# Kernel tuning notes

Hardware: AMD Instinct MI355X
Metric: run time of the kernel (lower is better)

The kernel has to match this reference:

```python
import jax, jax.numpy as jnp
import numpy as np

N = 100000      # nodes
E = 800000      # edges (avg degree 8)
F = 5           # num_node_features
D = 128         # embed_dim
H = 4           # heads
HD = D // H     # per-head dim = 32
H1, H2 = 64, 128  # mlp hidden dims


def _mlp(x, W1, b1, W2, b2, W3, b3):
    h = jax.nn.relu(x @ W1 + b1)
    h = jax.nn.relu(h @ W2 + b2)
    return h @ W3 + b3


def setup_inputs() -> dict:
    key = jax.random.key(0)
    ks = jax.random.split(key, 24)
    g = lambda i, shape: (jax.random.normal(ks[i], shape, dtype=jnp.float32) * 0.05)
    z = lambda d: jnp.zeros((d,), dtype=jnp.float32)
    return {
        "x": jax.random.normal(ks[0], (N, F), dtype=jnp.float32),
        "edge_index": jax.random.randint(ks[1], (2, E), 0, N),
        # mlp_prep: F -> 64 -> 128 -> D
        "prep_W1": g(2, (F, H1)),  "prep_b1": z(H1),
        "prep_W2": g(3, (H1, H2)), "prep_b2": z(H2),
        "prep_W3": g(4, (H2, D)),  "prep_b3": z(D),
        # mlp_update: D -> 64 -> 128 -> D
        "upd_W1": g(5, (D, H1)),   "upd_b1": z(H1),
        "upd_W2": g(6, (H1, H2)),  "upd_b2": z(H2),
        "upd_W3": g(7, (H2, D)),   "upd_b3": z(D),
        # TransformerConv projections (heads=4, per-head 32, concat -> D)
        "q_W": g(8, (D, D)),  "q_b": z(D),
        "k_W": g(9, (D, D)),  "k_b": z(D),
        "v_W": g(10, (D, D)), "v_b": z(D),
        "skip_W": g(11, (D, D)), "skip_b": z(D),
    }


def _transformer_conv(x, edge_index, q_W, q_b, k_W, k_b, v_W, v_b, skip_W, skip_b):
    # PyG TransformerConv: messages flow src=edge_index[0] -> dst=edge_index[1]
    src, dst = edge_index[0], edge_index[1]
    q = (x @ q_W + q_b).reshape(N, H, HD)
    k = (x @ k_W + k_b).reshape(N, H, HD)
    v = (x @ v_W + v_b).reshape(N, H, HD)
    scale = 1.0 / np.sqrt(HD).astype(np.float32)
    # per-edge attention logits [E, H]
    score = jnp.einsum('ehd,ehd->eh', q[dst], k[src]) * scale
    # segment softmax over incoming edges of each destination node
    m = jax.ops.segment_max(score, dst, num_segments=N)          # [N, H]
    e = jnp.exp(score - m[dst])                                  # [E, H]
    denom = jax.ops.segment_sum(e, dst, num_segments=N)         # [N, H]
    alpha = e / denom[dst]                                       # [E, H]
    # scatter-aggregate weighted values
    agg = jax.ops.segment_sum(alpha[..., None] * v[src], dst, num_segments=N)  # [N, H, HD]
    return agg.reshape(N, H * HD) + (x @ skip_W + skip_b)


def reference(x, edge_index,
              prep_W1, prep_b1, prep_W2, prep_b2, prep_W3, prep_b3,
              upd_W1, upd_b1, upd_W2, upd_b2, upd_W3, upd_b3,
              q_W, q_b, k_W, k_b, v_W, v_b, skip_W, skip_b):
    h_init = _mlp(x, prep_W1, prep_b1, prep_W2, prep_b2, prep_W3, prep_b3)
    h = _transformer_conv(h_init, edge_index, q_W, q_b, k_W, k_b, v_W, v_b, skip_W, skip_b)
    return h + _mlp(h, upd_W1, upd_b1, upd_W2, upd_b2, upd_W3, upd_b3)
```

## Files before the change

### kernel.cpp

```cpp
#include <hip/hip_runtime.h>
#include <hip/hip_bf16.h>

#define N_  100000
#define F_  5
#define D_  128
#define H_  4
#define HD_ 32
#define E_  800000

typedef __attribute__((ext_vector_type(8))) short bf16x8;
typedef __attribute__((ext_vector_type(4))) float f32x4;

__device__ __forceinline__ unsigned short f2bf(float f) {
  unsigned u = __float_as_uint(f);
  u += 0x7FFF + ((u >> 16) & 1);
  return (unsigned short)(u >> 16);
}

__device__ __forceinline__ unsigned pk2(float a, float b) {
  __hip_bfloat162 h = __float22bfloat162_rn(make_float2(a, b));
  return *(unsigned*)&h;
}

__device__ __forceinline__ float2 bf2f2(unsigned u) {
  float2 r;
  r.x = __uint_as_float(u << 16);
  r.y = __uint_as_float(u & 0xffff0000u);
  return r;
}

__device__ __forceinline__ float rowsum8(float x) {
  x += __int_as_float(__builtin_amdgcn_update_dpp(0, __float_as_int(x), 0x0B1, 0xF, 0xF, false));
  x += __int_as_float(__builtin_amdgcn_update_dpp(0, __float_as_int(x), 0x04E, 0xF, 0xF, false));
  x += __int_as_float(__builtin_amdgcn_update_dpp(0, __float_as_int(x), 0x141, 0xF, 0xF, false));
  return x;
}

template<int K, int M>
__device__ __forceinline__ void wconv_one(const float* __restrict__ W,
                                          unsigned short* __restrict__ WT,
                                          int idx) {
  const int r = idx & 7;
  const int l = (idx >> 3) & 15;
  const int rest = idx >> 7;
  const int kq = rest % (K / 8);
  const int i  = rest / (K / 8);
  WT[idx] = f2bf(W[(kq * 8 + r) * M + i * 16 + l]);
}

#define WCONV_NB 480
#define SCAN_NB ((N_ + 255) / 256)

__global__ __launch_bounds__(256) void k_wconv_all(
    const float* __restrict__ w0, const float* __restrict__ w1,
    const float* __restrict__ w2, const float* __restrict__ w3,
    const float* __restrict__ w4, const float* __restrict__ w5,
    const float* __restrict__ w6, const float* __restrict__ w7,
    const float* __restrict__ w8, unsigned short* __restrict__ WT,
    int* __restrict__ deg)
{
  if (blockIdx.x >= WCONV_NB) {
    const int i = (blockIdx.x - WCONV_NB) * 256 + threadIdx.x;
    if (i < N_) deg[i] = 0;
    return;
  }
  const int idx = blockIdx.x * 256 + threadIdx.x;
  if (idx < 8192)        wconv_one<64, 128>(w0, WT,          idx);
  else if (idx < 24576)  wconv_one<128,128>(w1, WT + 8192,   idx - 8192);
  else if (idx < 40960)  wconv_one<128,128>(w2, WT + 24576,  idx - 24576);
  else if (idx < 57344)  wconv_one<128,128>(w3, WT + 40960,  idx - 40960);
  else if (idx < 73728)  wconv_one<128,128>(w4, WT + 57344,  idx - 57344);
  else if (idx < 90112)  wconv_one<128,128>(w5, WT + 73728,  idx - 73728);
  else if (idx < 98304)  wconv_one<128, 64>(w6, WT + 90112,  idx - 90112);
  else if (idx < 106496) wconv_one<64, 128>(w7, WT + 98304,  idx - 98304);
  else                   wconv_one<128,128>(w8, WT + 106496, idx - 106496);
}

template<int K, int M>
__device__ __forceinline__ void gemm_frag(const unsigned short* sX,
                                          const unsigned short* __restrict__ WT,
                                          f32x4 (*acc)[4],
                                          int wr, int wc, int l16, int kg)
{
  constexpr int SX = K + 8;
  constexpr int IF = M / 32;
  #pragma unroll
  for (int i = 0; i < IF; ++i)
    #pragma unroll
    for (int j = 0; j < 4; ++j) acc[i][j] = (f32x4){0.f, 0.f, 0.f, 0.f};
  #pragma unroll
  for (int k0 = 0; k0 < K; k0 += 32) {
    const int kq = k0 / 8 + kg;
    bf16x8 aw[IF];
    #pragma unroll
    for (int i = 0; i < IF; ++i)
      aw[i] = *(const bf16x8*)&WT[(((wr * IF + i) * (K / 8) + kq) * 16 + l16) * 8];
    #pragma unroll
    for (int j = 0; j < 4; ++j) {
      const bf16x8 bx = *(const bf16x8*)&sX[(wc * 64 + j * 16 + l16) * SX + k0 + kg * 8];
      #pragma unroll
      for (int i = 0; i < IF; ++i)
        acc[i][j] = __builtin_amdgcn_mfma_f32_16x16x32_bf16(aw[i], bx, acc[i][j], 0, 0, 0);
    }
  }
}

template<int M, bool RELU, int SXO>
__device__ __forceinline__ void acc_to_lds(unsigned short* sY, f32x4 (*acc)[4],
                                           const float* __restrict__ bias,
                                           int wr, int wc, int l16, int kg)
{
  constexpr int IF = M / 32;
  float4 b4[IF];
  #pragma unroll
  for (int i = 0; i < IF; ++i)
    b4[i] = *(const float4*)&bias[(wr * IF + i) * 16 + kg * 4];
  #pragma unroll
  for (int j = 0; j < 4; ++j) {
    const int row = wc * 64 + j * 16 + l16;
    #pragma unroll
    for (int i = 0; i < IF; ++i) {
      const int f0 = (wr * IF + i) * 16 + kg * 4;
      float ox = acc[i][j][0] + b4[i].x, oy = acc[i][j][1] + b4[i].y;
      float oz = acc[i][j][2] + b4[i].z, ow = acc[i][j][3] + b4[i].w;
      if constexpr (RELU) {
        ox = fmaxf(ox, 0.f); oy = fmaxf(oy, 0.f);
        oz = fmaxf(oz, 0.f); ow = fmaxf(ow, 0.f);
      }
      uint2 p;
      p.x = pk2(ox, oy);
      p.y = pk2(oz, ow);
      *(uint2*)&sY[row * SXO + f0] = p;
    }
  }
}

__global__ __launch_bounds__(256) void k_prep_proj(
    const float* __restrict__ x,
    const float* __restrict__ pW1, const float* __restrict__ pb1,
    const unsigned short* __restrict__ wt_p2, const float* __restrict__ pb2,
    const unsigned short* __restrict__ wt_p3, const float* __restrict__ pb3,
    const unsigned short* __restrict__ wt_q, const float* __restrict__ qb,
    const unsigned short* __restrict__ wt_k, const float* __restrict__ kb,
    const unsigned short* __restrict__ wt_v, const float* __restrict__ vb,
    const unsigned short* __restrict__ wt_s, const float* __restrict__ sb,
    unsigned short* __restrict__ q16, unsigned short* __restrict__ k16,
    unsigned short* __restrict__ v16, float* __restrict__ out)
{
  __shared__ __align__(16) unsigned short bufA[128 * 72];
  __shared__ __align__(16) unsigned short bufB[128 * 136];

  const int t = threadIdx.x;
  const int node0 = blockIdx.x * 128;
  const int lane = t & 63;
  const int w  = t >> 6;
  const int wr = w >> 1, wc = w & 1;
  const int l16 = lane & 15, kg = lane >> 4;

  float* sxs = (float*)bufB;
  float* sw1 = (float*)bufB + 640;
  {
    const long gbase = (long)node0 * F_;
    for (int i = t; i < 128 * F_; i += 256) {
      const long g = gbase + i;
      sxs[i] = (g < (long)N_ * F_) ? x[g] : 0.f;
    }
    for (int i = t; i < 384; i += 256)
      sw1[i] = (i < 320) ? pW1[i] : pb1[i - 320];
  }
  __syncthreads();

  {
    const int n = t >> 1;
    const int half = (t & 1) * 32;
    float xr[F_];
    #pragma unroll
    for (int k = 0; k < F_; ++k) xr[k] = sxs[n * F_ + k];
    const float* sb1 = sw1 + 320;
    #pragma unroll
    for (int q = 0; q < 8; ++q) {
      float o[4];
      #pragma unroll
      for (int jj = 0; jj < 4; ++jj) {
        const int f = half + q * 4 + jj;
        float a = sb1[f];
        #pragma unroll
        for (int k = 0; k < F_; ++k) a = fmaf(xr[k], sw1[k * 64 + f], a);
        o[jj] = fmaxf(a, 0.f);
      }
      uint2 pkd;
      pkd.x = pk2(o[0], o[1]);
      pkd.y = pk2(o[2], o[3]);
      *(uint2*)&bufA[n * 72 + half + q * 4] = pkd;
    }
  }
  __syncthreads();

  f32x4 acc[4][4];

  gemm_frag<64, 128>(bufA, wt_p2, acc, wr, wc, l16, kg);
  acc_to_lds<128, true, 136>(bufB, acc, pb2, wr, wc, l16, kg);
  __syncthreads();

  gemm_frag<128, 128>(bufB, wt_p3, acc, wr, wc, l16, kg);
  __syncthreads();
  acc_to_lds<128, false, 136>(bufB, acc, pb3, wr, wc, l16, kg);
  __syncthreads();

  {
    const unsigned short* wtsP[3] = {wt_q, wt_k, wt_v};
    const float* bsP[3] = {qb, kb, vb};
    unsigned short* ysP[3] = {q16, k16, v16};
    #pragma unroll
    for (int ws = 0; ws < 3; ++ws) {
      gemm_frag<128, 128>(bufB, wtsP[ws], acc, wr, wc, l16, kg);
      const float* __restrict__ bias = bsP[ws];
      unsigned short* __restrict__ Yb = ysP[ws];
      float4 b4[4];
      #pragma unroll
      for (int i = 0; i < 4; ++i)
        b4[i] = *(const float4*)&bias[(wr * 4 + i) * 16 + kg * 4];
      #pragma unroll
      for (int j = 0; j < 4; ++j) {
        const int node = node0 + wc * 64 + j * 16 + l16;
        if (node >= N_) continue;
        #pragma unroll
        for (int i = 0; i < 4; ++i) {
          const int f0 = (wr * 4 + i) * 16 + kg * 4;
          uint2 ob;
          ob.x = pk2(acc[i][j][0] + b4[i].x, acc[i][j][1] + b4[i].y);
          ob.y = pk2(acc[i][j][2] + b4[i].z, acc[i][j][3] + b4[i].w);
          *(uint2*)&Yb[(long)node * D_ + f0] = ob;
        }
      }
    }
  }

  gemm_frag<128, 128>(bufB, wt_s, acc, wr, wc, l16, kg);
  {
    float4 b4[4];
    #pragma unroll
    for (int i = 0; i < 4; ++i)
      b4[i] = *(const float4*)&sb[(wr * 4 + i) * 16 + kg * 4];
    #pragma unroll
    for (int j = 0; j < 4; ++j) {
      const int node = node0 + wc * 64 + j * 16 + l16;
      if (node >= N_) continue;
      #pragma unroll
      for (int i = 0; i < 4; ++i) {
        const int f0 = (wr * 4 + i) * 16 + kg * 4;
        float4 o = make_float4(acc[i][j][0] + b4[i].x, acc[i][j][1] + b4[i].y,
                               acc[i][j][2] + b4[i].z, acc[i][j][3] + b4[i].w);
        *(float4*)&out[(long)node * D_ + f0] = o;
      }
    }
  }
}

__global__ __launch_bounds__(256) void k_update(
    const unsigned short* __restrict__ wt_u1, const float* __restrict__ ub1,
    const unsigned short* __restrict__ wt_u2, const float* __restrict__ ub2,
    const unsigned short* __restrict__ wt_u3, const float* __restrict__ ub3,
    float* __restrict__ out)
{
  __shared__ __align__(16) unsigned short bufA[128 * 72];
  __shared__ __align__(16) unsigned short bufB[128 * 136];

  const int t = threadIdx.x;
  const int node0 = blockIdx.x * 128;
  const int lane = t & 63;
  const int w  = t >> 6;
  const int wr = w >> 1, wc = w & 1;
  const int l16 = lane & 15, kg = lane >> 4;

  #pragma unroll
  for (int i = 0; i < 16; ++i) {
    const int g = t + 256 * i;
    const int row = g >> 5;
    const int kc  = g & 31;
    const int node = node0 + row;
    float4 xv = (node < N_) ? ((const float4*)out)[(long)node * 32 + kc]
                            : make_float4(0.f, 0.f, 0.f, 0.f);
    uint2 p;
    p.x = pk2(xv.x, xv.y);
    p.y = pk2(xv.z, xv.w);
    *(uint2*)&bufB[row * 136 + kc * 4] = p;
  }
  __syncthreads();

  f32x4 acc[4][4];

  gemm_frag<128, 64>(bufB, wt_u1, acc, wr, wc, l16, kg);
  acc_to_lds<64, true, 72>(bufA, acc, ub1, wr, wc, l16, kg);
  __syncthreads();

  gemm_frag<64, 128>(bufA, wt_u2, acc, wr, wc, l16, kg);
  acc_to_lds<128, true, 136>(bufB, acc, ub2, wr, wc, l16, kg);
  __syncthreads();

  gemm_frag<128, 128>(bufB, wt_u3, acc, wr, wc, l16, kg);
  {
    float4 b4[4];
    #pragma unroll
    for (int i = 0; i < 4; ++i)
      b4[i] = *(const float4*)&ub3[(wr * 4 + i) * 16 + kg * 4];
    #pragma unroll
    for (int j = 0; j < 4; ++j) {
      const int node = node0 + wc * 64 + j * 16 + l16;
      if (node >= N_) continue;
      #pragma unroll
      for (int i = 0; i < 4; ++i) {
        const int f0 = (wr * 4 + i) * 16 + kg * 4;
        const float4 r = *(const float4*)&out[(long)node * D_ + f0];
        float4 o = make_float4(acc[i][j][0] + b4[i].x + r.x,
                               acc[i][j][1] + b4[i].y + r.y,
                               acc[i][j][2] + b4[i].z + r.z,
                               acc[i][j][3] + b4[i].w + r.w);
        *(float4*)&out[(long)node * D_ + f0] = o;
      }
    }
  }
}

__global__ __launch_bounds__(256) void k_hist(const int* __restrict__ ei,
                                              int* __restrict__ deg) {
  int e = blockIdx.x * 256 + threadIdx.x;
  if (e < E_) atomicAdd(&deg[ei[E_ + e]], 1);
}

__global__ __launch_bounds__(256) void k_scan1(const int* __restrict__ deg,
                                               int* __restrict__ off,
                                               int* __restrict__ bsum) {
  __shared__ int s[256];
  const int t = threadIdx.x;
  const int i = blockIdx.x * 256 + t;
  const int v = (i < N_) ? deg[i] : 0;
  s[t] = v;
  __syncthreads();
  #pragma unroll
  for (int o = 1; o < 256; o <<= 1) {
    int u = (t >= o) ? s[t - o] : 0;
    __syncthreads();
    s[t] += u;
    __syncthreads();
  }
  if (i < N_) off[i] = s[t] - v;
  if (t == 255) bsum[blockIdx.x] = s[255];
}

__global__ __launch_bounds__(256) void k_scan23(const int* __restrict__ off,
                                                const int* __restrict__ bsum,
                                                int* __restrict__ cur,
                                                const int* __restrict__ deg,
                                                int2* __restrict__ meta) {
  __shared__ int sacc[256];
  const int t = threadIdx.x;
  const int bid = blockIdx.x;
  int s = 0;
  for (int j = t; j < bid; j += 256) s += bsum[j];
  sacc[t] = s;
  __syncthreads();
  #pragma unroll
  for (int o = 128; o > 0; o >>= 1) {
    if (t < o) sacc[t] += sacc[t + o];
    __syncthreads();
  }
  const int prefix = sacc[0];
  const int i = bid * 256 + t;
  if (i < N_) {
    const int o = off[i] + prefix;
    cur[i] = o;
    meta[i] = make_int2(o, deg[i]);
  }
}

__global__ __launch_bounds__(256) void k_fill(const int* __restrict__ ei,
                                              int* __restrict__ cur,
                                              int* __restrict__ esrc) {
  int e = blockIdx.x * 256 + threadIdx.x;
  if (e < E_) {
    int src = ei[e], dst = ei[E_ + e];
    int pos = atomicAdd(&cur[dst], 1);
    esrc[pos] = src;
  }
}

__global__ __launch_bounds__(256) void k_attn(
    const int* __restrict__ esrc, const int2* __restrict__ meta,
    const unsigned short* __restrict__ q,
    const unsigned short* __restrict__ kbuf,
    const unsigned short* __restrict__ vbuf,
    float* __restrict__ out)
{
  const int node = blockIdx.x * 4 + (threadIdx.x >> 6);
  const int lane = threadIdx.x & 63;
  if (node >= N_) return;

  const int2 md = meta[node];
  const int start = md.x, cnt = md.y;
  const int end = start + cnt;
  const int h = lane >> 5;
  const int c = lane & 31;
  const float C = 0.17677669529663687f * 1.4426950408889634f;

  const uint2 qu = *(const uint2*)&q[((unsigned)node << 7) + 4u * c];
  const float2 q01 = bf2f2(qu.x), q23 = bf2f2(qu.y);
  const float qx0 = q01.x * C, qx1 = q01.y * C;
  const float qx2 = q23.x * C, qx3 = q23.y * C;

  float l = 0.f, a0 = 0.f, a1 = 0.f, a2 = 0.f, a3 = 0.f;

  const int P = (cnt + 3) >> 2;
  if (P > 0) {
    int eA = start + 2 * h, eB = eA + 1;
    bool vAc = eA < end, vBc = eB < end;
    unsigned iA = esrc[vAc ? eA : start];
    unsigned iB = esrc[vBc ? eB : start];
    uint2 kA = *(const uint2*)&kbuf[(iA << 7) + 4u * c];
    uint2 kB = *(const uint2*)&kbuf[(iB << 7) + 4u * c];
    uint2 wA = *(const uint2*)&vbuf[(iA << 7) + 4u * c];
    uint2 wB = *(const uint2*)&vbuf[(iB << 7) + 4u * c];
    int eA1 = eA + 4, eB1 = eB + 4;
    bool vA1 = eA1 < end, vB1 = eB1 < end;
    unsigned iA1 = esrc[vA1 ? eA1 : start];
    unsigned iB1 = esrc[vB1 ? eB1 : start];

    for (int it = 0;;) {
      const bool more = (it + 1) < P;
      uint2 kAn, kBn, wAn, wBn;
      unsigned iA2 = 0, iB2 = 0;
      bool vA2 = false, vB2 = false;
      if (more) {
        kAn = *(const uint2*)&kbuf[(iA1 << 7) + 4u * c];
        kBn = *(const uint2*)&kbuf[(iB1 << 7) + 4u * c];
        wAn = *(const uint2*)&vbuf[(iA1 << 7) + 4u * c];
        wBn = *(const uint2*)&vbuf[(iB1 << 7) + 4u * c];
        const int eA2 = start + 4 * (it + 2) + 2 * h;
        const int eB2 = eA2 + 1;
        vA2 = eA2 < end; vB2 = eB2 < end;
        iA2 = esrc[vA2 ? eA2 : start];
        iB2 = esrc[vB2 ? eB2 : start];
      }

      const float2 ka01 = bf2f2(kA.x), ka23 = bf2f2(kA.y);
      const float2 kb01 = bf2f2(kB.x), kb23 = bf2f2(kB.y);
      float sA = fmaf(qx0, ka01.x, fmaf(qx1, ka01.y, fmaf(qx2, ka23.x, qx3 * ka23.y)));
      float sB = fmaf(qx0, kb01.x, fmaf(qx1, kb01.y, fmaf(qx2, kb23.x, qx3 * kb23.y)));
      sA = rowsum8(sA);
      sB = rowsum8(sB);
      const float eAe = vAc ? __builtin_amdgcn_exp2f(sA) : 0.f;
      const float eBe = vBc ? __builtin_amdgcn_exp2f(sB) : 0.f;
      const float2 va01 = bf2f2(wA.x), va23 = bf2f2(wA.y);
      const float2 vb01 = bf2f2(wB.x), vb23 = bf2f2(wB.y);
      l += eAe + eBe;
      a0 = fmaf(eAe, va01.x, fmaf(eBe, vb01.x, a0));
      a1 = fmaf(eAe, va01.y, fmaf(eBe, vb01.y, a1));
      a2 = fmaf(eAe, va23.x, fmaf(eBe, vb23.x, a2));
      a3 = fmaf(eAe, va23.y, fmaf(eBe, vb23.y, a3));

      if (!more) break;
      ++it;
      kA = kAn; kB = kBn; wA = wAn; wB = wBn;
      vAc = vA1; vBc = vB1;
      vA1 = vA2; vB1 = vB2;
      iA1 = iA2; iB1 = iB2;
    }
  }

  l  += __shfl_xor(l, 32);
  a0 += __shfl_xor(a0, 32);
  a1 += __shfl_xor(a1, 32);
  a2 += __shfl_xor(a2, 32);
  a3 += __shfl_xor(a3, 32);

  if (h == 0 && l > 0.f) {
    const float inv = 1.0f / l;
    float4* op = (float4*)&out[((unsigned)node << 7) + 4u * c];
    float4 cv = *op;
    cv.x += a0 * inv;
    cv.y += a1 * inv;
    cv.z += a2 * inv;
    cv.w += a3 * inv;
    *op = cv;
  }
}

extern "C" void kernel_launch(void* const* d_in, const int* in_sizes, int n_in,
                              void* d_out, int out_size, void* d_ws, size_t ws_size,
                              hipStream_t stream) {
  const float* x   = (const float*)d_in[0];
  const int*   ei  = (const int*)d_in[1];
  const float* pW1 = (const float*)d_in[2];  const float* pb1 = (const float*)d_in[3];
  const float* pW2 = (const float*)d_in[4];  const float* pb2 = (const float*)d_in[5];
  const float* pW3 = (const float*)d_in[6];  const float* pb3 = (const float*)d_in[7];
  const float* uW1 = (const float*)d_in[8];  const float* ub1 = (const float*)d_in[9];
  const float* uW2 = (const float*)d_in[10]; const float* ub2 = (const float*)d_in[11];
  const float* uW3 = (const float*)d_in[12]; const float* ub3 = (const float*)d_in[13];
  const float* qW  = (const float*)d_in[14]; const float* qb  = (const float*)d_in[15];
  const float* kW  = (const float*)d_in[16]; const float* kb  = (const float*)d_in[17];
  const float* vW  = (const float*)d_in[18]; const float* vb  = (const float*)d_in[19];
  const float* sW  = (const float*)d_in[20]; const float* sb  = (const float*)d_in[21];

  float* out = (float*)d_out;
  float* ws  = (float*)d_ws;

  const long ND = (long)N_ * D_;
  unsigned short* q16 = (unsigned short*)(ws + ND);
  unsigned short* k16 = (unsigned short*)(ws + 2 * ND);
  unsigned short* v16 = (unsigned short*)(ws + 3 * ND);

  unsigned short* wtb = (unsigned short*)(ws + 4 * ND);
  unsigned short* wt_p2 = wtb;
  unsigned short* wt_p3 = wtb + 8192;
  unsigned short* wt_q  = wtb + 24576;
  unsigned short* wt_k  = wtb + 40960;
  unsigned short* wt_v  = wtb + 57344;
  unsigned short* wt_s  = wtb + 73728;
  unsigned short* wt_u1 = wtb + 90112;
  unsigned short* wt_u2 = wtb + 98304;
  unsigned short* wt_u3 = wtb + 106496;

  int* deg  = (int*)ws;
  int* off  = deg + N_;
  int* cur  = off + N_;
  int* esrc = cur + N_;
  int* bsum = esrc + E_;
  int2* meta = (int2*)(bsum + 512);

  const int gT = (N_ + 127) / 128;

  k_wconv_all<<<WCONV_NB + SCAN_NB, 256, 0, stream>>>(
      pW2, pW3, qW, kW, vW, sW, uW1, uW2, uW3, wtb, deg);

  k_hist  <<<(E_ + 255) / 256, 256, 0, stream>>>(ei, deg);
  k_scan1 <<<SCAN_NB, 256, 0, stream>>>(deg, off, bsum);
  k_scan23<<<SCAN_NB, 256, 0, stream>>>(off, bsum, cur, deg, meta);
  k_fill  <<<(E_ + 255) / 256, 256, 0, stream>>>(ei, cur, esrc);

  k_prep_proj<<<gT, 256, 0, stream>>>(
      x, pW1, pb1, wt_p2, pb2, wt_p3, pb3,
      wt_q, qb, wt_k, kb, wt_v, vb, wt_s, sb,
      q16, k16, v16, out);

  k_attn<<<(N_ + 3) / 4, 256, 0, stream>>>(esrc, meta, q16, k16, v16, out);

  k_update<<<gT, 256, 0, stream>>>(wt_u1, ub1, wt_u2, ub2, wt_u3, ub3, out);
}
```

Measured before the change: 366.2 us.

## Map two nodes per wave in attention with a persistent grid-stride loop

The attention kernel now assigns each half-wave its own destination node instead of splitting one node's edges across both half-waves, which removes the final cross-half shuffle reduction. It also launches a fixed grid of 2048 blocks that loop over node pairs in grid-stride fashion instead of one wave per node. This aims to cut per-node setup overhead and improve lane utilisation for low-degree nodes. The trade-off is longer serial edge chains per half-wave and more load imbalance when node degrees vary.

```diff
diff --git a/kernel.cpp b/kernel.cpp
--- a/kernel.cpp
+++ b/kernel.cpp
@@ -385,6 +385,8 @@
   }
 }
 
+#define ATTN_NB 2048
+
 __global__ __launch_bounds__(256) void k_attn(
     const int* __restrict__ esrc, const int2* __restrict__ meta,
     const unsigned short* __restrict__ q,
@@ -392,96 +394,90 @@
     const unsigned short* __restrict__ vbuf,
     float* __restrict__ out)
 {
-  const int node = blockIdx.x * 4 + (threadIdx.x >> 6);
   const int lane = threadIdx.x & 63;
-  if (node >= N_) return;
-
-  const int2 md = meta[node];
-  const int start = md.x, cnt = md.y;
-  const int end = start + cnt;
   const int h = lane >> 5;
   const int c = lane & 31;
+  const int gwave = (blockIdx.x << 2) + (threadIdx.x >> 6);
+  const int NWAVE = ATTN_NB * 4;
   const float C = 0.17677669529663687f * 1.4426950408889634f;
 
-  const uint2 qu = *(const uint2*)&q[((unsigned)node << 7) + 4u * c];
-  const float2 q01 = bf2f2(qu.x), q23 = bf2f2(qu.y);
-  const float qx0 = q01.x * C, qx1 = q01.y * C;
-  const float qx2 = q23.x * C, qx3 = q23.y * C;
-
-  float l = 0.f, a0 = 0.f, a1 = 0.f, a2 = 0.f, a3 = 0.f;
-
-  const int P = (cnt + 3) >> 2;
-  if (P > 0) {
-    int eA = start + 2 * h, eB = eA + 1;
-    bool vAc = eA < end, vBc = eB < end;
-    unsigned iA = esrc[vAc ? eA : start];
-    unsigned iB = esrc[vBc ? eB : start];
-    uint2 kA = *(const uint2*)&kbuf[(iA << 7) + 4u * c];
-    uint2 kB = *(const uint2*)&kbuf[(iB << 7) + 4u * c];
-    uint2 wA = *(const uint2*)&vbuf[(iA << 7) + 4u * c];
-    uint2 wB = *(const uint2*)&vbuf[(iB << 7) + 4u * c];
-    int eA1 = eA + 4, eB1 = eB + 4;
-    bool vA1 = eA1 < end, vB1 = eB1 < end;
-    unsigned iA1 = esrc[vA1 ? eA1 : start];
-    unsigned iB1 = esrc[vB1 ? eB1 : start];
-
-    for (int it = 0;;) {
-      const bool more = (it + 1) < P;
-      uint2 kAn, kBn, wAn, wBn;
-      unsigned iA2 = 0, iB2 = 0;
-      bool vA2 = false, vB2 = false;
-      if (more) {
-        kAn = *(const uint2*)&kbuf[(iA1 << 7) + 4u * c];
-        kBn = *(const uint2*)&kbuf[(iB1 << 7) + 4u * c];
-        wAn = *(const uint2*)&vbuf[(iA1 << 7) + 4u * c];
-        wBn = *(const uint2*)&vbuf[(iB1 << 7) + 4u * c];
-        const int eA2 = start + 4 * (it + 2) + 2 * h;
-        const int eB2 = eA2 + 1;
-        vA2 = eA2 < end; vB2 = eB2 < end;
-        iA2 = esrc[vA2 ? eA2 : start];
-        iB2 = esrc[vB2 ? eB2 : start];
+  for (int pair = gwave; 2 * pair < N_; pair += NWAVE) {
+    const unsigned node = 2 * pair + h;
+    const int2 md = meta[node];
+    const int start = md.x, cnt = md.y;
+    const int end = start + cnt;
+
+    const uint2 qu = *(const uint2*)&q[(node << 7) + 4u * c];
+    const float2 q01 = bf2f2(qu.x), q23 = bf2f2(qu.y);
+    const float qx0 = q01.x * C, qx1 = q01.y * C;
+    const float qx2 = q23.x * C, qx3 = q23.y * C;
+
+    float l = 0.f, a0 = 0.f, a1 = 0.f, a2 = 0.f, a3 = 0.f;
+
+    const int P = (cnt + 1) >> 1;
+    if (P > 0) {
+      bool v1c = (start + 1) < end;
+      unsigned i0 = esrc[start];
+      unsigned i1 = esrc[v1c ? start + 1 : start];
+      uint2 kA = *(const uint2*)&kbuf[(i0 << 7) + 4u * c];
+      uint2 kB = *(const uint2*)&kbuf[(i1 << 7) + 4u * c];
+      uint2 wA = *(const uint2*)&vbuf[(i0 << 7) + 4u * c];
+      uint2 wB = *(const uint2*)&vbuf[(i1 << 7) + 4u * c];
+      bool v0n = (start + 2) < end, v1n = (start + 3) < end;
+      unsigned i0n = esrc[v0n ? start + 2 : start];
+      unsigned i1n = esrc[v1n ? start + 3 : start];
+
+      for (int it = 0;;) {
+        const bool more = (it + 1) < P;
+        uint2 kAn, kBn, wAn, wBn;
+        unsigned i0f = 0, i1f = 0;
+        bool v0f = false, v1f = false;
+        if (more) {
+          kAn = *(const uint2*)&kbuf[(i0n << 7) + 4u * c];
+          kBn = *(const uint2*)&kbuf[(i1n << 7) + 4u * c];
+          wAn = *(const uint2*)&vbuf[(i0n << 7) + 4u * c];
+          wBn = *(const uint2*)&vbuf[(i1n << 7) + 4u * c];
+          const int ef = start + 2 * (it + 2);
+          v0f = ef < end; v1f = (ef + 1) < end;
+          i0f = esrc[v0f ? ef : start];
+          i1f = esrc[v1f ? ef + 1 : start];
+        }
+
+        const float2 ka01 = bf2f2(kA.x), ka23 = bf2f2(kA.y);
+        const float2 kb01 = bf2f2(kB.x), kb23 = bf2f2(kB.y);
+        float sA = fmaf(qx0, ka01.x, fmaf(qx1, ka01.y, fmaf(qx2, ka23.x, qx3 * ka23.y)));
+        float sB = fmaf(qx0, kb01.x, fmaf(qx1, kb01.y, fmaf(qx2, kb23.x, qx3 * kb23.y)));
+        sA = rowsum8(sA);
+        sB = rowsum8(sB);
+        const float eA = __builtin_amdgcn_exp2f(sA);
+        const float eB = v1c ? __builtin_amdgcn_exp2f(sB) : 0.f;
+        const float2 va01 = bf2f2(wA.x), va23 = bf2f2(wA.y);
+        const float2 vb01 = bf2f2(wB.x), vb23 = bf2f2(wB.y);
+        l += eA + eB;
+        a0 = fmaf(eA, va01.x, fmaf(eB, vb01.x, a0));
+        a1 = fmaf(eA, va01.y, fmaf(eB, vb01.y, a1));
+        a2 = fmaf(eA, va23.x, fmaf(eB, vb23.x, a2));
+        a3 = fmaf(eA, va23.y, fmaf(eB, vb23.y, a3));
+
+        if (!more) break;
+        ++it;
+        kA = kAn; kB = kBn; wA = wAn; wB = wBn;
+        v1c = v1n;
+        v0n = v0f; v1n = v1f;
+        i0n = i0f; i1n = i1f;
       }
-
-      const float2 ka01 = bf2f2(kA.x), ka23 = bf2f2(kA.y);
-      const float2 kb01 = bf2f2(kB.x), kb23 = bf2f2(kB.y);
-      float sA = fmaf(qx0, ka01.x, fmaf(qx1, ka01.y, fmaf(qx2, ka23.x, qx3 * ka23.y)));
-      float sB = fmaf(qx0, kb01.x, fmaf(qx1, kb01.y, fmaf(qx2, kb23.x, qx3 * kb23.y)));
-      sA = rowsum8(sA);
-      sB = rowsum8(sB);
-      const float eAe = vAc ? __builtin_amdgcn_exp2f(sA) : 0.f;
-      const float eBe = vBc ? __builtin_amdgcn_exp2f(sB) : 0.f;
-      const float2 va01 = bf2f2(wA.x), va23 = bf2f2(wA.y);
-      const float2 vb01 = bf2f2(wB.x), vb23 = bf2f2(wB.y);
-      l += eAe + eBe;
-      a0 = fmaf(eAe, va01.x, fmaf(eBe, vb01.x, a0));
-      a1 = fmaf(eAe, va01.y, fmaf(eBe, vb01.y, a1));
-      a2 = fmaf(eAe, va23.x, fmaf(eBe, vb23.x, a2));
-      a3 = fmaf(eAe, va23.y, fmaf(eBe, vb23.y, a3));
-
-      if (!more) break;
-      ++it;
-      kA = kAn; kB = kBn; wA = wAn; wB = wBn;
-      vAc = vA1; vBc = vB1;
-      vA1 = vA2; vB1 = vB2;
-      iA1 = iA2; iB1 = iB2;
-    }
-  }
-
-  l  += __shfl_xor(l, 32);
-  a0 += __shfl_xor(a0, 32);
-  a1 += __shfl_xor(a1, 32);
-  a2 += __shfl_xor(a2, 32);
-  a3 += __shfl_xor(a3, 32);
-
-  if (h == 0 && l > 0.f) {
-    const float inv = 1.0f / l;
-    float4* op = (float4*)&out[((unsigned)node << 7) + 4u * c];
-    float4 cv = *op;
-    cv.x += a0 * inv;
-    cv.y += a1 * inv;
-    cv.z += a2 * inv;
-    cv.w += a3 * inv;
-    *op = cv;
+    }
+
+    if (l > 0.f) {
+      const float inv = 1.0f / l;
+      float4* op = (float4*)&out[(node << 7) + 4u * c];
+      float4 cv = *op;
+      cv.x += a0 * inv;
+      cv.y += a1 * inv;
+      cv.z += a2 * inv;
+      cv.w += a3 * inv;
+      *op = cv;
+    }
   }
 }
 
@@ -542,7 +538,7 @@
       wt_q, qb, wt_k, kb, wt_v, vb, wt_s, sb,
       q16, k16, v16, out);
 
-  k_attn<<<(N_ + 3) / 4, 256, 0, stream>>>(esrc, meta, q16, k16, v16, out);
+  k_attn<<<ATTN_NB, 256, 0, stream>>>(esrc, meta, q16, k16, v16, out);
 
   k_update<<<gT, 256, 0, stream>>>(wt_u1, ub1, wt_u2, ub2, wt_u3, ub3, out);
 }
```

After: 370.5 us. Within noise of the previous version (+1.2%).
